# Performance work log

Hardware: AMD Instinct MI355X
Metric: run time of the kernel (lower is better)

The kernel has to match this reference:

```python
import jax, jax.numpy as jnp
import numpy as np

N = 4096
NODE_DIM = 256
HIDDEN = 64
N_CLASSES = 16
N_HEADS = 4
NEG_SLOPE = 0.01  # F.leaky_relu default


def _xavier(key, shape):
    fan_out, fan_in = shape[0], shape[1]
    limit = float(np.sqrt(6.0 / (fan_in + fan_out)))
    return jax.random.uniform(key, shape, jnp.float32, -limit, limit)


def setup_inputs() -> dict:
    key = jax.random.key(0)
    ks = jax.random.split(key, 8)
    x = jax.random.normal(ks[0], (N, NODE_DIM), jnp.float32)
    adj_mat = jax.random.randint(ks[1], (N, N), 0, 2, jnp.int32)
    # head-stacked layer-1 params
    W1 = _xavier(ks[2], (N_HEADS * HIDDEN, NODE_DIM)).reshape(N_HEADS, HIDDEN, NODE_DIM)
    a1_1 = _xavier(ks[3], (N_HEADS * HIDDEN, 1)).reshape(N_HEADS, HIDDEN)
    a2_1 = _xavier(ks[4], (N_HEADS * HIDDEN, 1)).reshape(N_HEADS, HIDDEN)
    # layer-2 params
    W2 = _xavier(ks[5], (N_CLASSES, N_HEADS * HIDDEN))
    a1_2 = _xavier(ks[6], (N_CLASSES, 1))[:, 0]
    a2_2 = _xavier(ks[7], (N_CLASSES, 1))[:, 0]
    return {"x": x, "adj_mat": adj_mat, "W1": W1, "a1_1": a1_1, "a2_1": a2_1,
            "W2": W2, "a1_2": a1_2, "a2_2": a2_2}


def _attention_layer(x, adj_f, W, a1, a2):
    # x: [N, in_dim], W: [out_dim, in_dim], a1/a2: [out_dim]
    h = x @ W.T                               # [N, d]
    f1 = h @ a1                               # [N]
    f2 = h @ a2                               # [N]
    e = jax.nn.leaky_relu(f1[:, None] + f2[None, :], NEG_SLOPE)  # [N, N]
    e = e * adj_f
    e = jnp.where(e == 0, -jnp.inf, e)        # faithful to torch.where(e==0, -inf, e)
    alpha = jax.nn.softmax(e, axis=1)         # [N, N]
    return alpha @ h                          # [N, d]


def reference(x, adj_mat, W1, a1_1, a2_1, W2, a1_2, a2_2):
    adj_f = adj_mat.astype(x.dtype)
    # layer 1: vmap over heads, concat along feature dim
    heads = jax.vmap(_attention_layer, in_axes=(None, None, 0, 0, 0))(
        x, adj_f, W1, a1_1, a2_1)              # [H, N, hidden]
    h = jnp.transpose(heads, (1, 0, 2)).reshape(N, N_HEADS * HIDDEN)
    h = jax.nn.elu(h)
    # dropout p=0.0 -> identity
    logits = _attention_layer(h, adj_f, W2, a1_2, a2_2)  # [N, n_classes]
    return logits
```

## Files before the change

kernel.cpp:

```cpp
#include <hip/hip_runtime.h>
#include <cstdint>

typedef __bf16 bf16x8 __attribute__((ext_vector_type(8)));
typedef float  f32x4  __attribute__((ext_vector_type(4)));

#define LOG2E 1.44269504088896f

__device__ __forceinline__ void split8(const float* v, bf16x8& hi, bf16x8& lo) {
    union { bf16x8 v; __bf16 e[8]; } h, l;
    #pragma unroll
    for (int j = 0; j < 8; j++) {
        __bf16 hb = (__bf16)v[j];
        float  r  = v[j] - (float)hb;
        h.e[j] = hb; l.e[j] = (__bf16)r;
    }
    hi = h.v; lo = l.v;
}
__device__ __forceinline__ bf16x8 cvt8(const float* v) {
    union { bf16x8 v; __bf16 e[8]; } u;
    #pragma unroll
    for (int j = 0; j < 8; j++) u.e[j] = (__bf16)v[j];
    return u.v;
}
__device__ __forceinline__ void splitstore(unsigned short* ph, unsigned short* pl, float v) {
    __bf16 hb = (__bf16)v;
    float  r  = v - (float)hb;
    __bf16 lb = (__bf16)r;
    unsigned short hu, lu;
    __builtin_memcpy(&hu, &hb, 2); __builtin_memcpy(&lu, &lb, 2);
    *ph = hu; *pl = lu;
}
__device__ __forceinline__ unsigned short f2bfh(float v) {
    __bf16 hb = (__bf16)v; unsigned short hu;
    __builtin_memcpy(&hu, &hb, 2); return hu;
}

__global__ __launch_bounds__(256)
void kzero(float4* __restrict__ p) {
    p[blockIdx.x * 256 + threadIdx.x] = float4{0.f, 0.f, 0.f, 0.f};
}

__global__ __launch_bounds__(256)
void kpre(const int* __restrict__ adj, unsigned long long* __restrict__ bm64,
          const float* __restrict__ w1, const float* __restrict__ w2,
          unsigned short* __restrict__ w1h, unsigned short* __restrict__ w1l,
          unsigned short* __restrict__ w2h, unsigned short* __restrict__ w2l) {
    int bx = blockIdx.x, tid = threadIdx.x;
    if (bx < 8192) {
        int row = bx >> 1, jbase = (bx & 1) * 2048;
        int wave = tid >> 6, lane = tid & 63;
        const int* base = adj + (size_t)row * 4096 + jbase + wave * 512;
        unsigned long long* bmw = bm64 + row * 64 + (jbase >> 6) + wave * 8;
        #pragma unroll
        for (int it = 0; it < 8; it++) {
            int v = base[it * 64 + lane];
            unsigned long long mask = __ballot(v != 0);
            if (lane == 0) bmw[it] = mask;
        }
        return;
    }
    int e = ((bx - 8192) * 256 + tid) * 4;
    const float* src; unsigned short *dh, *dl;
    if (e < 65536) { src = w1 + e; dh = w1h + e; dl = w1l + e; }
    else { int e2 = e - 65536; src = w2 + e2; dh = w2h + e2; dl = w2l + e2; }
    #pragma unroll
    for (int j = 0; j < 4; j++) splitstore(dh + j, dl + j, src[j]);
}

__global__ __launch_bounds__(256)
void k1_gemm(const float* __restrict__ x,
             const unsigned short* __restrict__ w1h,
             const unsigned short* __restrict__ w1l,
             const float* __restrict__ a11, const float* __restrict__ a21,
             unsigned short* __restrict__ h1t_hi, float* __restrict__ fvals) {
    int tid = threadIdx.x, wave = tid >> 6, lane = tid & 63;
    int q = lane >> 4, m = lane & 15;
    int i0 = blockIdx.x * 16;
    int c0 = wave * 64;
    f32x4 acc[4] = {};
    #pragma unroll
    for (int k0 = 0; k0 < 256; k0 += 32) {
        bf16x8 ah, al;
        split8(x + (i0 + m) * 256 + k0 + q * 8, ah, al);
        #pragma unroll
        for (int ct = 0; ct < 4; ct++) {
            bf16x8 bh = *(const bf16x8*)(w1h + (c0 + ct * 16 + m) * 256 + k0 + q * 8);
            bf16x8 bl = *(const bf16x8*)(w1l + (c0 + ct * 16 + m) * 256 + k0 + q * 8);
            acc[ct] = __builtin_amdgcn_mfma_f32_16x16x32_bf16(ah, bh, acc[ct], 0, 0, 0);
            acc[ct] = __builtin_amdgcn_mfma_f32_16x16x32_bf16(al, bh, acc[ct], 0, 0, 0);
            acc[ct] = __builtin_amdgcn_mfma_f32_16x16x32_bf16(ah, bl, acc[ct], 0, 0, 0);
        }
    }
    float a1v[4], a2v[4];
    #pragma unroll
    for (int ct = 0; ct < 4; ct++) {
        a1v[ct] = a11[wave * 64 + ct * 16 + m];
        a2v[ct] = a21[wave * 64 + ct * 16 + m];
    }
    #pragma unroll
    for (int r = 0; r < 4; r++) {
        int i = i0 + q * 4 + r;
        float s1 = 0.f, s2 = 0.f;
        #pragma unroll
        for (int ct = 0; ct < 4; ct++) {
            int c = c0 + ct * 16 + m;
            h1t_hi[c * 4096 + i] = f2bfh(acc[ct][r]);
            s1 += acc[ct][r] * a1v[ct];
            s2 += acc[ct][r] * a2v[ct];
        }
        #pragma unroll
        for (int off = 1; off < 16; off <<= 1) {
            s1 += __shfl_xor(s1, off);
            s2 += __shfl_xor(s2, off);
        }
        if (m == 0) {
            fvals[wave * 4096 + i] = s1 * LOG2E;
            fvals[16384 + wave * 4096 + i] = s2 * LOG2E;
        }
    }
}

template<int NCT, int JLEN, bool ATOM>
__global__ __launch_bounds__(256)
void attn_kernel(const unsigned char* __restrict__ bmb,
                 const float* __restrict__ f1_all,
                 const float* __restrict__ f2_all,
                 const unsigned short* __restrict__ BTh_all,
                 float* __restrict__ pacc,
                 float* __restrict__ zacc,
                 int pstride) {
    constexpr int S    = JLEN / 32;
    constexpr int ST   = (S % 8 == 0) ? S + 4 : S;
    constexpr int PR   = S / 4;
    constexpr int NU4  = 128 * PR;
    constexpr int CR   = NCT * 16;
    constexpr int TSTR = 40;
    int tid = threadIdx.x, wave = tid >> 6, lane = tid & 63;
    int q = lane >> 4, m = lane & 15;
    int head = blockIdx.y;
    int i0 = blockIdx.x * 128;
    int jstart = blockIdx.z * JLEN;

    if (!ATOM) {
        pacc += (size_t)blockIdx.z * (size_t)(4096 * pstride);
        zacc += (size_t)blockIdx.z * (size_t)((NCT == 4 ? 4 : 1) * 4096);
    }

    __shared__ unsigned int ldsbm[128 * ST];
    __shared__ unsigned short ldsbt[2][CR * TSTR];

    const unsigned short* BTh = BTh_all + (size_t)head * CR * 4096;

    for (int c = tid; c < NU4; c += 256) {
        int row = c / PR, part = c % PR;
        uint4 v = *(const uint4*)(bmb + (size_t)(i0 + row) * 512 + (jstart >> 3) + part * 16);
        *(uint4*)&ldsbm[row * ST + part * 4] = v;
    }
    uint4 vstage;
    int sc = tid >> 2, sp = tid & 3;
    if (tid < CR * 4) {
        vstage = *(const uint4*)(BTh + (size_t)sc * 4096 + jstart + sp * 8);
        *(uint4*)&ldsbt[0][sc * TSTR + sp * 8] = vstage;
    }

    const float* f1 = f1_all + head * 4096;
    const float* f2 = f2_all + head * 4096;
    int col0 = head * CR;

    int r0 = wave * 32;
    float f1s0 = f1[i0 + r0 + m];
    float f1s1 = f1[i0 + r0 + 16 + m];

    bf16x8 bones;
    {
        union { bf16x8 v; unsigned short u[8]; } t;
        unsigned short one = (m == 0) ? 0x3F80 : 0;
        #pragma unroll
        for (int j = 0; j < 8; j++) t.u[j] = one;
        bones = t.v;
    }

    f32x4 acc0[NCT] = {}, acc1[NCT] = {};
    f32x4 accz0 = {}, accz1 = {};

    constexpr int NIT = JLEN / 32;
    for (int it = 0; it < NIT; it++) {
        __syncthreads();
        int jl = it * 32;
        if (it + 1 < NIT && tid < CR * 4)
            vstage = *(const uint4*)(BTh + (size_t)sc * 4096 + jstart + jl + 32 + sp * 8);

        unsigned int md0 = ldsbm[(r0 + m) * ST + (jl >> 5)];
        unsigned int md1 = ldsbm[(r0 + 16 + m) * ST + (jl >> 5)];
        const float4* f2p = (const float4*)(f2 + jstart + jl + q * 8);
        float4 fa = f2p[0], fb = f2p[1];
        float fv[8] = {fa.x, fa.y, fa.z, fa.w, fb.x, fb.y, fb.z, fb.w};
        float pv0[8], pv1[8];
        #pragma unroll
        for (int jj = 0; jj < 8; jj++) {
            int bit = q * 8 + jj;
            float s0 = f1s0 + fv[jj];
            float e0 = fmaxf(s0, 0.01f * s0);
            bool v0 = ((md0 >> bit) & 1u) && (s0 != 0.0f);
            float p0 = v0 ? __builtin_exp2f(e0) : 0.0f;
            pv0[jj] = p0;
            float s1 = f1s1 + fv[jj];
            float e1 = fmaxf(s1, 0.01f * s1);
            bool v1 = ((md1 >> bit) & 1u) && (s1 != 0.0f);
            float p1 = v1 ? __builtin_exp2f(e1) : 0.0f;
            pv1[jj] = p1;
        }
        bf16x8 ah0 = cvt8(pv0), ah1 = cvt8(pv1);
        int cur = it & 1;
        #pragma unroll
        for (int ct = 0; ct < NCT; ct++) {
            bf16x8 bh = *(const bf16x8*)&ldsbt[cur][(ct * 16 + m) * TSTR + q * 8];
            acc0[ct] = __builtin_amdgcn_mfma_f32_16x16x32_bf16(ah0, bh, acc0[ct], 0, 0, 0);
            acc1[ct] = __builtin_amdgcn_mfma_f32_16x16x32_bf16(ah1, bh, acc1[ct], 0, 0, 0);
        }
        accz0 = __builtin_amdgcn_mfma_f32_16x16x32_bf16(ah0, bones, accz0, 0, 0, 0);
        accz1 = __builtin_amdgcn_mfma_f32_16x16x32_bf16(ah1, bones, accz1, 0, 0, 0);
        if (it + 1 < NIT && tid < CR * 4)
            *(uint4*)&ldsbt[1 - cur][sc * TSTR + sp * 8] = vstage;
    }
    if (m == 0) {
        #pragma unroll
        for (int r = 0; r < 4; r++) {
            int rowA = i0 + r0 + q * 4 + r;
            if (ATOM) {
                atomicAdd(&zacc[head * 4096 + rowA], accz0[r]);
                atomicAdd(&zacc[head * 4096 + rowA + 16], accz1[r]);
            } else {
                zacc[head * 4096 + rowA] = accz0[r];
                zacc[head * 4096 + rowA + 16] = accz1[r];
            }
        }
    }
    #pragma unroll
    for (int ct = 0; ct < NCT; ct++)
        #pragma unroll
        for (int r = 0; r < 4; r++) {
            int col = col0 + ct * 16 + m;
            int rowA = i0 + r0 + q * 4 + r;
            if (ATOM) {
                atomicAdd(&pacc[rowA * pstride + col], acc0[ct][r]);
                atomicAdd(&pacc[(rowA + 16) * pstride + col], acc1[ct][r]);
            } else {
                pacc[rowA * pstride + col] = acc0[ct][r];
                pacc[(rowA + 16) * pstride + col] = acc1[ct][r];
            }
        }
}

__global__ __launch_bounds__(256)
void fin1c(const float* __restrict__ pp, const float* __restrict__ zp, int nj,
           unsigned short* __restrict__ hh, unsigned short* __restrict__ hl) {
    int row = blockIdx.x, col = threadIdx.x;
    float s = 0.f;
    for (int jc = 0; jc < nj; jc++) s += pp[(size_t)jc * (4096 * 256) + row * 256 + col];
    int head = col >> 6;
    float zz = 0.f;
    for (int jc = 0; jc < nj; jc++) zz += zp[jc * (4 * 4096) + head * 4096 + row];
    float v = s / zz;
    v = (v > 0.f) ? v : (__expf(v) - 1.0f);
    splitstore(&hh[row * 256 + col], &hl[row * 256 + col], v);
}

__global__ __launch_bounds__(256)
void k3_layer2(const unsigned short* __restrict__ helu_hi,
               const unsigned short* __restrict__ helu_lo,
               const unsigned short* __restrict__ w2h,
               const unsigned short* __restrict__ w2l,
               const float* __restrict__ a12,
               const float* __restrict__ a22,
               unsigned short* __restrict__ h2t_hi,
               float* __restrict__ fq) {
    int tid = threadIdx.x, wave = tid >> 6, lane = tid & 63;
    int q = lane >> 4, m = lane & 15;
    int i0 = (blockIdx.x * 4 + wave) * 16;
    f32x4 acc = {};
    #pragma unroll
    for (int k0 = 0; k0 < 256; k0 += 32) {
        bf16x8 ah = *(const bf16x8*)(helu_hi + (i0 + m) * 256 + k0 + q * 8);
        bf16x8 al = *(const bf16x8*)(helu_lo + (i0 + m) * 256 + k0 + q * 8);
        bf16x8 bh = *(const bf16x8*)(w2h + m * 256 + k0 + q * 8);
        bf16x8 bl = *(const bf16x8*)(w2l + m * 256 + k0 + q * 8);
        acc = __builtin_amdgcn_mfma_f32_16x16x32_bf16(ah, bh, acc, 0, 0, 0);
        acc = __builtin_amdgcn_mfma_f32_16x16x32_bf16(al, bh, acc, 0, 0, 0);
        acc = __builtin_amdgcn_mfma_f32_16x16x32_bf16(ah, bl, acc, 0, 0, 0);
    }
    float a1v = a12[m], a2v = a22[m];
    #pragma unroll
    for (int r = 0; r < 4; r++) {
        float v = acc[r];
        int i = i0 + q * 4 + r;
        h2t_hi[m * 4096 + i] = f2bfh(v);
        float s1 = v * a1v, s2 = v * a2v;
        #pragma unroll
        for (int off = 1; off < 16; off <<= 1) {
            s1 += __shfl_xor(s1, off);
            s2 += __shfl_xor(s2, off);
        }
        if (m == 0) { fq[i] = s1 * LOG2E; fq[4096 + i] = s2 * LOG2E; }
    }
}

__global__ __launch_bounds__(256)
void fin2(const float* __restrict__ pp, const float* __restrict__ zp, int nj,
          float* __restrict__ out) {
    int idx = blockIdx.x * 256 + threadIdx.x;
    float s = 0.f;
    for (int jc = 0; jc < nj; jc++) s += pp[jc * 65536 + idx];
    float zz = 0.f;
    for (int jc = 0; jc < nj; jc++) zz += zp[jc * 4096 + (idx >> 4)];
    out[idx] = s / zz;
}

extern "C" void kernel_launch(void* const* d_in, const int* in_sizes, int n_in,
                              void* d_out, int out_size, void* d_ws, size_t ws_size,
                              hipStream_t stream) {
    const float* x   = (const float*)d_in[0];
    const int*   adj = (const int*)d_in[1];
    const float* w1  = (const float*)d_in[2];
    const float* a11 = (const float*)d_in[3];
    const float* a21 = (const float*)d_in[4];
    const float* w2  = (const float*)d_in[5];
    const float* a12 = (const float*)d_in[6];
    const float* a22 = (const float*)d_in[7];
    float* out = (float*)d_out;

    uint8_t* w = (uint8_t*)d_ws;
    unsigned long long* bm  = (unsigned long long*)(w);
    unsigned short* h1t_hi  = (unsigned short*)(w + (2u << 20));
    unsigned short* h2t_hi  = (unsigned short*)(w + (4u << 20));
    float*          fvals   = (float*)(w + (4u << 20) + (128u << 10));
    float*          fq      = (float*)(w + (4u << 20) + (256u << 10));
    unsigned short* w1h     = (unsigned short*)(w + (4u << 20) + (288u << 10));
    unsigned short* w1l     = (unsigned short*)(w + (4u << 20) + (416u << 10));
    unsigned short* w2h     = (unsigned short*)(w + (4u << 20) + (544u << 10));
    unsigned short* w2l     = (unsigned short*)(w + (4u << 20) + (552u << 10));
    unsigned short* helu_hi = (unsigned short*)(w + (4u << 20) + (560u << 10));
    unsigned short* helu_lo = (unsigned short*)(w + (4u << 20) + (2608u << 10));

    bool big = ws_size >= ((size_t)48 << 20);
    float* p1 = (float*)(w + (9u << 20));
    float *z1, *p2, *z2;
    if (big) {
        z1 = p1 + (size_t)8 * 4096 * 256;
        p2 = z1 + 8 * 4 * 4096;
        z2 = p2 + (size_t)16 * 4096 * 16;
    } else {
        z1 = p1 + 4096 * 256;
        p2 = z1 + 4 * 4096;
        z2 = p2 + 4096 * 16;
    }

    if (!big) kzero<<<1108, 256, 0, stream>>>((float4*)p1);
    kpre<<<8260, 256, 0, stream>>>(adj, bm, w1, w2, w1h, w1l, w2h, w2l);
    k1_gemm<<<256, 256, 0, stream>>>(x, w1h, w1l, a11, a21, h1t_hi, fvals);
    if (big)
        attn_kernel<4, 512, false><<<dim3(32, 4, 8), 256, 0, stream>>>(
            (const unsigned char*)bm, fvals, fvals + 16384, h1t_hi, p1, z1, 256);
    else
        attn_kernel<4, 512, true><<<dim3(32, 4, 8), 256, 0, stream>>>(
            (const unsigned char*)bm, fvals, fvals + 16384, h1t_hi, p1, z1, 256);
    fin1c<<<4096, 256, 0, stream>>>(p1, z1, big ? 8 : 1, helu_hi, helu_lo);
    k3_layer2<<<64, 256, 0, stream>>>(helu_hi, helu_lo, w2h, w2l, a12, a22,
                                      h2t_hi, fq);
    if (big)
        attn_kernel<1, 256, false><<<dim3(32, 1, 16), 256, 0, stream>>>(
            (const unsigned char*)bm, fq, fq + 4096, h2t_hi, p2, z2, 16);
    else
        attn_kernel<1, 256, true><<<dim3(32, 1, 16), 256, 0, stream>>>(
            (const unsigned char*)bm, fq, fq + 4096, h2t_hi, p2, z2, 16);
    fin2<<<256, 256, 0, stream>>>(p2, z2, big ? 16 : 1, out);
}
```

Measured before the change: 208.2 us.

## Factor leaky-relu exponent into rank-1 terms to remove per-element exp

New measurement: 214.6 us. 1.03x slower.

```diff
diff --git a/kernel.cpp b/kernel.cpp
--- a/kernel.cpp
+++ b/kernel.cpp
@@ -3,8 +3,6 @@
 
 typedef __bf16 bf16x8 __attribute__((ext_vector_type(8)));
 typedef float  f32x4  __attribute__((ext_vector_type(4)));
-
-#define LOG2E 1.44269504088896f
 
 __device__ __forceinline__ void split8(const float* v, bf16x8& hi, bf16x8& lo) {
     union { bf16x8 v; __bf16 e[8]; } h, l;
@@ -15,12 +13,6 @@
         h.e[j] = hb; l.e[j] = (__bf16)r;
     }
     hi = h.v; lo = l.v;
-}
-__device__ __forceinline__ bf16x8 cvt8(const float* v) {
-    union { bf16x8 v; __bf16 e[8]; } u;
-    #pragma unroll
-    for (int j = 0; j < 8; j++) u.e[j] = (__bf16)v[j];
-    return u.v;
 }
 __device__ __forceinline__ void splitstore(unsigned short* ph, unsigned short* pl, float v) {
     __bf16 hb = (__bf16)v;
@@ -72,7 +64,10 @@
              const unsigned short* __restrict__ w1h,
              const unsigned short* __restrict__ w1l,
              const float* __restrict__ a11, const float* __restrict__ a21,
-             unsigned short* __restrict__ h1t_hi, float* __restrict__ fvals) {
+             unsigned short* __restrict__ h1t_hi,
+             float* __restrict__ f2f, float* __restrict__ nf,
+             float* __restrict__ ue, float* __restrict__ ae,
+             unsigned short* __restrict__ vb, unsigned short* __restrict__ bb) {
     int tid = threadIdx.x, wave = tid >> 6, lane = tid & 63;
     int q = lane >> 4, m = lane & 15;
     int i0 = blockIdx.x * 16;
@@ -114,8 +109,13 @@
             s2 += __shfl_xor(s2, off);
         }
         if (m == 0) {
-            fvals[wave * 4096 + i] = s1 * LOG2E;
-            fvals[16384 + wave * 4096 + i] = s2 * LOG2E;
+            int idx = wave * 4096 + i;
+            f2f[idx] = s2;
+            nf[idx]  = -s1;
+            ue[idx]  = __expf(s1);
+            ae[idx]  = __expf(0.01f * s1);
+            vb[idx]  = f2bfh(__expf(s2));
+            bb[idx]  = f2bfh(__expf(0.01f * s2));
         }
     }
 }
@@ -123,8 +123,12 @@
 template<int NCT, int JLEN, bool ATOM>
 __global__ __launch_bounds__(256)
 void attn_kernel(const unsigned char* __restrict__ bmb,
-                 const float* __restrict__ f1_all,
-                 const float* __restrict__ f2_all,
+                 const float* __restrict__ f2f_all,
+                 const float* __restrict__ nf_all,
+                 const float* __restrict__ ue_all,
+                 const float* __restrict__ ae_all,
+                 const unsigned short* __restrict__ vb_all,
+                 const unsigned short* __restrict__ bb_all,
                  const unsigned short* __restrict__ BTh_all,
                  float* __restrict__ pacc,
                  float* __restrict__ zacc,
@@ -163,13 +167,14 @@
         *(uint4*)&ldsbt[0][sc * TSTR + sp * 8] = vstage;
     }
 
-    const float* f1 = f1_all + head * 4096;
-    const float* f2 = f2_all + head * 4096;
+    const float* f2f = f2f_all + head * 4096;
+    const unsigned short* vb = vb_all + head * 4096;
+    const unsigned short* bb = bb_all + head * 4096;
     int col0 = head * CR;
 
     int r0 = wave * 32;
-    float f1s0 = f1[i0 + r0 + m];
-    float f1s1 = f1[i0 + r0 + 16 + m];
+    float nfa = nf_all[head * 4096 + i0 + r0 + m];
+    float nfb = nf_all[head * 4096 + i0 + r0 + 16 + m];
 
     bf16x8 bones;
     {
@@ -180,8 +185,8 @@
         bones = t.v;
     }
 
-    f32x4 acc0[NCT] = {}, acc1[NCT] = {};
-    f32x4 accz0 = {}, accz1 = {};
+    f32x4 acc1a[NCT] = {}, acc2a[NCT] = {}, acc1b[NCT] = {}, acc2b[NCT] = {};
+    f32x4 z1a = {}, z2a = {}, z1b = {}, z2b = {};
 
     constexpr int NIT = JLEN / 32;
     for (int it = 0; it < NIT; it++) {
@@ -192,64 +197,72 @@
 
         unsigned int md0 = ldsbm[(r0 + m) * ST + (jl >> 5)];
         unsigned int md1 = ldsbm[(r0 + 16 + m) * ST + (jl >> 5)];
-        const float4* f2p = (const float4*)(f2 + jstart + jl + q * 8);
+        const float4* f2p = (const float4*)(f2f + jstart + jl + q * 8);
         float4 fa = f2p[0], fb = f2p[1];
         float fv[8] = {fa.x, fa.y, fa.z, fa.w, fb.x, fb.y, fb.z, fb.w};
-        float pv0[8], pv1[8];
+        union { bf16x8 v; unsigned short u[8]; } vbu, bbu, A1a, A2a, A1b, A2b;
+        vbu.v = *(const bf16x8*)(vb + jstart + jl + q * 8);
+        bbu.v = *(const bf16x8*)(bb + jstart + jl + q * 8);
         #pragma unroll
         for (int jj = 0; jj < 8; jj++) {
             int bit = q * 8 + jj;
-            float s0 = f1s0 + fv[jj];
-            float e0 = fmaxf(s0, 0.01f * s0);
-            bool v0 = ((md0 >> bit) & 1u) && (s0 != 0.0f);
-            float p0 = v0 ? __builtin_exp2f(e0) : 0.0f;
-            pv0[jj] = p0;
-            float s1 = f1s1 + fv[jj];
-            float e1 = fmaxf(s1, 0.01f * s1);
-            bool v1 = ((md1 >> bit) & 1u) && (s1 != 0.0f);
-            float p1 = v1 ? __builtin_exp2f(e1) : 0.0f;
-            pv1[jj] = p1;
-        }
-        bf16x8 ah0 = cvt8(pv0), ah1 = cvt8(pv1);
+            float f = fv[jj];
+            bool nz0 = ((md0 >> bit) & 1u) && (f != nfa);
+            bool nz1 = ((md1 >> bit) & 1u) && (f != nfb);
+            bool p0 = f > nfa;
+            bool p1 = f > nfb;
+            A1a.u[jj] = (nz0 && p0)  ? vbu.u[jj] : (unsigned short)0;
+            A2a.u[jj] = (nz0 && !p0) ? bbu.u[jj] : (unsigned short)0;
+            A1b.u[jj] = (nz1 && p1)  ? vbu.u[jj] : (unsigned short)0;
+            A2b.u[jj] = (nz1 && !p1) ? bbu.u[jj] : (unsigned short)0;
+        }
         int cur = it & 1;
         #pragma unroll
         for (int ct = 0; ct < NCT; ct++) {
             bf16x8 bh = *(const bf16x8*)&ldsbt[cur][(ct * 16 + m) * TSTR + q * 8];
-            acc0[ct] = __builtin_amdgcn_mfma_f32_16x16x32_bf16(ah0, bh, acc0[ct], 0, 0, 0);
-            acc1[ct] = __builtin_amdgcn_mfma_f32_16x16x32_bf16(ah1, bh, acc1[ct], 0, 0, 0);
-        }
-        accz0 = __builtin_amdgcn_mfma_f32_16x16x32_bf16(ah0, bones, accz0, 0, 0, 0);
-        accz1 = __builtin_amdgcn_mfma_f32_16x16x32_bf16(ah1, bones, accz1, 0, 0, 0);
+            acc1a[ct] = __builtin_amdgcn_mfma_f32_16x16x32_bf16(A1a.v, bh, acc1a[ct], 0, 0, 0);
+            acc2a[ct] = __builtin_amdgcn_mfma_f32_16x16x32_bf16(A2a.v, bh, acc2a[ct], 0, 0, 0);
+            acc1b[ct] = __builtin_amdgcn_mfma_f32_16x16x32_bf16(A1b.v, bh, acc1b[ct], 0, 0, 0);
+            acc2b[ct] = __builtin_amdgcn_mfma_f32_16x16x32_bf16(A2b.v, bh, acc2b[ct], 0, 0, 0);
+        }
+        z1a = __builtin_amdgcn_mfma_f32_16x16x32_bf16(A1a.v, bones, z1a, 0, 0, 0);
+        z2a = __builtin_amdgcn_mfma_f32_16x16x32_bf16(A2a.v, bones, z2a, 0, 0, 0);
+        z1b = __builtin_amdgcn_mfma_f32_16x16x32_bf16(A1b.v, bones, z1b, 0, 0, 0);
+        z2b = __builtin_amdgcn_mfma_f32_16x16x32_bf16(A2b.v, bones, z2b, 0, 0, 0);
         if (it + 1 < NIT && tid < CR * 4)
             *(uint4*)&ldsbt[1 - cur][sc * TSTR + sp * 8] = vstage;
     }
-    if (m == 0) {
-        #pragma unroll
-        for (int r = 0; r < 4; r++) {
-            int rowA = i0 + r0 + q * 4 + r;
+    #pragma unroll
+    for (int r = 0; r < 4; r++) {
+        int rowA = i0 + r0 + q * 4 + r;
+        int rowB = rowA + 16;
+        float uA = ue_all[head * 4096 + rowA], aA = ae_all[head * 4096 + rowA];
+        float uB = ue_all[head * 4096 + rowB], aB = ae_all[head * 4096 + rowB];
+        if (m == 0) {
+            float za = uA * z1a[r] + aA * z2a[r];
+            float zb = uB * z1b[r] + aB * z2b[r];
             if (ATOM) {
-                atomicAdd(&zacc[head * 4096 + rowA], accz0[r]);
-                atomicAdd(&zacc[head * 4096 + rowA + 16], accz1[r]);
+                atomicAdd(&zacc[head * 4096 + rowA], za);
+                atomicAdd(&zacc[head * 4096 + rowB], zb);
             } else {
-                zacc[head * 4096 + rowA] = accz0[r];
-                zacc[head * 4096 + rowA + 16] = accz1[r];
+                zacc[head * 4096 + rowA] = za;
+                zacc[head * 4096 + rowB] = zb;
             }
         }
-    }
-    #pragma unroll
-    for (int ct = 0; ct < NCT; ct++)
-        #pragma unroll
-        for (int r = 0; r < 4; r++) {
+        #pragma unroll
+        for (int ct = 0; ct < NCT; ct++) {
             int col = col0 + ct * 16 + m;
-            int rowA = i0 + r0 + q * 4 + r;
+            float vA = uA * acc1a[ct][r] + aA * acc2a[ct][r];
+            float vB = uB * acc1b[ct][r] + aB * acc2b[ct][r];
             if (ATOM) {
-                atomicAdd(&pacc[rowA * pstride + col], acc0[ct][r]);
-                atomicAdd(&pacc[(rowA + 16) * pstride + col], acc1[ct][r]);
+                atomicAdd(&pacc[rowA * pstride + col], vA);
+                atomicAdd(&pacc[rowB * pstride + col], vB);
             } else {
-                pacc[rowA * pstride + col] = acc0[ct][r];
-                pacc[(rowA + 16) * pstride + col] = acc1[ct][r];
+                pacc[rowA * pstride + col] = vA;
+                pacc[rowB * pstride + col] = vB;
             }
         }
+    }
 }
 
 __global__ __launch_bounds__(256)
@@ -274,7 +287,9 @@
                const float* __restrict__ a12,
                const float* __restrict__ a22,
                unsigned short* __restrict__ h2t_hi,
-               float* __restrict__ fq) {
+               float* __restrict__ f2f, float* __restrict__ nf,
+               float* __restrict__ ue, float* __restrict__ ae,
+               unsigned short* __restrict__ vb, unsigned short* __restrict__ bb) {
     int tid = threadIdx.x, wave = tid >> 6, lane = tid & 63;
     int q = lane >> 4, m = lane & 15;
     int i0 = (blockIdx.x * 4 + wave) * 16;
@@ -301,7 +316,14 @@
             s1 += __shfl_xor(s1, off);
             s2 += __shfl_xor(s2, off);
         }
-        if (m == 0) { fq[i] = s1 * LOG2E; fq[4096 + i] = s2 * LOG2E; }
+        if (m == 0) {
+            f2f[i] = s2;
+            nf[i]  = -s1;
+            ue[i]  = __expf(s1);
+            ae[i]  = __expf(0.01f * s1);
+            vb[i]  = f2bfh(__expf(s2));
+            bb[i]  = f2bfh(__expf(0.01f * s2));
+        }
     }
 }
 
@@ -333,14 +355,24 @@
     unsigned long long* bm  = (unsigned long long*)(w);
     unsigned short* h1t_hi  = (unsigned short*)(w + (2u << 20));
     unsigned short* h2t_hi  = (unsigned short*)(w + (4u << 20));
-    float*          fvals   = (float*)(w + (4u << 20) + (128u << 10));
-    float*          fq      = (float*)(w + (4u << 20) + (256u << 10));
-    unsigned short* w1h     = (unsigned short*)(w + (4u << 20) + (288u << 10));
-    unsigned short* w1l     = (unsigned short*)(w + (4u << 20) + (416u << 10));
-    unsigned short* w2h     = (unsigned short*)(w + (4u << 20) + (544u << 10));
-    unsigned short* w2l     = (unsigned short*)(w + (4u << 20) + (552u << 10));
-    unsigned short* helu_hi = (unsigned short*)(w + (4u << 20) + (560u << 10));
-    unsigned short* helu_lo = (unsigned short*)(w + (4u << 20) + (2608u << 10));
+    unsigned short* w1h     = (unsigned short*)(w + (4u << 20) + (128u << 10));
+    unsigned short* w1l     = (unsigned short*)(w + (4u << 20) + (256u << 10));
+    unsigned short* w2h     = (unsigned short*)(w + (4u << 20) + (384u << 10));
+    unsigned short* w2l     = (unsigned short*)(w + (4u << 20) + (392u << 10));
+    float*          f2f1    = (float*)(w + (4u << 20) + (400u << 10));
+    float*          nf1a    = (float*)(w + (4u << 20) + (464u << 10));
+    float*          ue1     = (float*)(w + (4u << 20) + (528u << 10));
+    float*          ae1     = (float*)(w + (4u << 20) + (592u << 10));
+    unsigned short* vb1     = (unsigned short*)(w + (4u << 20) + (656u << 10));
+    unsigned short* bb1     = (unsigned short*)(w + (4u << 20) + (688u << 10));
+    float*          f2f2    = (float*)(w + (4u << 20) + (720u << 10));
+    float*          nf2a    = (float*)(w + (4u << 20) + (736u << 10));
+    float*          ue2     = (float*)(w + (4u << 20) + (752u << 10));
+    float*          ae2     = (float*)(w + (4u << 20) + (768u << 10));
+    unsigned short* vb2     = (unsigned short*)(w + (4u << 20) + (784u << 10));
+    unsigned short* bb2     = (unsigned short*)(w + (4u << 20) + (792u << 10));
+    unsigned short* helu_hi = (unsigned short*)(w + (4u << 20) + (800u << 10));
+    unsigned short* helu_lo = (unsigned short*)(w + (4u << 20) + (2848u << 10));
 
     bool big = ws_size >= ((size_t)48 << 20);
     float* p1 = (float*)(w + (9u << 20));
@@ -357,21 +389,26 @@
 
     if (!big) kzero<<<1108, 256, 0, stream>>>((float4*)p1);
     kpre<<<8260, 256, 0, stream>>>(adj, bm, w1, w2, w1h, w1l, w2h, w2l);
-    k1_gemm<<<256, 256, 0, stream>>>(x, w1h, w1l, a11, a21, h1t_hi, fvals);
+    k1_gemm<<<256, 256, 0, stream>>>(x, w1h, w1l, a11, a21, h1t_hi,
+                                     f2f1, nf1a, ue1, ae1, vb1, bb1);
     if (big)
         attn_kernel<4, 512, false><<<dim3(32, 4, 8), 256, 0, stream>>>(
-            (const unsigned char*)bm, fvals, fvals + 16384, h1t_hi, p1, z1, 256);
+            (const unsigned char*)bm, f2f1, nf1a, ue1, ae1, vb1, bb1,
+            h1t_hi, p1, z1, 256);
     else
         attn_kernel<4, 512, true><<<dim3(32, 4, 8), 256, 0, stream>>>(
-            (const unsigned char*)bm, fvals, fvals + 16384, h1t_hi, p1, z1, 256);
+            (const unsigned char*)bm, f2f1, nf1a, ue1, ae1, vb1, bb1,
+            h1t_hi, p1, z1, 256);
     fin1c<<<4096, 256, 0, stream>>>(p1, z1, big ? 8 : 1, helu_hi, helu_lo);
     k3_layer2<<<64, 256, 0, stream>>>(helu_hi, helu_lo, w2h, w2l, a12, a22,
-                                      h2t_hi, fq);
+                                      h2t_hi, f2f2, nf2a, ue2, ae2, vb2, bb2);
     if (big)
         attn_kernel<1, 256, false><<<dim3(32, 1, 16), 256, 0, stream>>>(
-            (const unsigned char*)bm, fq, fq + 4096, h2t_hi, p2, z2, 16);
+            (const unsigned char*)bm, f2f2, nf2a, ue2, ae2, vb2, bb2,
+            h2t_hi, p2, z2, 16);
     else
         attn_kernel<1, 256, true><<<dim3(32, 1, 16), 256, 0, stream>>>(
-            (const unsigned char*)bm, fq, fq + 4096, h2t_hi, p2, z2, 16);
+            (const unsigned char*)bm, f2f2, nf2a, ue2, ae2, vb2, bb2,
+            h2t_hi, p2, z2, 16);
     fin2<<<256, 256, 0, stream>>>(p2, z2, big ? 16 : 1, out);
 }
```
